# Kernel tuning notes

Measured on AMD Instinct MI355X. Metric: run time of the kernel, lower is better.

Reference implementation:

```python
import jax, jax.numpy as jnp
import numpy as np

LEVELS = 100
TIMESTAMPS = 32768
DIM = 2048
N = 32768
SIG_MIN, SIG_MAX = -3.0, 3.0


def _bipolar(key, shape):
    return jnp.where(jax.random.uniform(key, shape) < 0.5, -1.0, 1.0).astype(jnp.float32)


def setup_inputs() -> dict:
    key = jax.random.key(0)
    ks = jax.random.split(key, 11)
    # (t, x, y, z): sorted times in [0, TIMESTAMPS), gaussian signals
    times = jnp.sort(jax.random.uniform(ks[0], (N,), minval=0.0, maxval=float(TIMESTAMPS)))
    # ensure strictly increasing so jerk dt != 0
    times = times + jnp.arange(N, dtype=jnp.float32) * 1e-3
    xyz = jax.random.normal(ks[1], (N, 3), dtype=jnp.float32)
    inp = jnp.concatenate([times[:, None], xyz], axis=1)  # [N,4]
    return {
        "input": inp,
        "W_x": _bipolar(ks[2], (LEVELS, DIM)),
        "W_y": _bipolar(ks[3], (LEVELS, DIM)),
        "W_z": _bipolar(ks[4], (LEVELS, DIM)),
        "W_mag": _bipolar(ks[5], (LEVELS, DIM)),
        "W_xj": _bipolar(ks[6], (LEVELS, DIM)),
        "W_yj": _bipolar(ks[7], (LEVELS, DIM)),
        "W_zj": _bipolar(ks[8], (LEVELS, DIM)),
        "W_magj": _bipolar(ks[9], (LEVELS, DIM)),
        "W_t": _bipolar(ks[10], (TIMESTAMPS, DIM)),
    }


def _level_lookup(table, value, low, high):
    # torchhd Level: map value in [low, high] to index in [0, n-1], clamp, gather
    n = table.shape[0]
    idx = jnp.round((value - low) / (high - low) * (n - 1)).astype(jnp.int32)
    idx = jnp.clip(idx, 0, n - 1)
    return table[idx]  # [N, DIM]


def reference(input, W_x, W_y, W_z, W_mag, W_xj, W_yj, W_zj, W_magj, W_t):
    t = input[:, 0] - input[0, 0]
    x = jnp.clip(input[:, 1], SIG_MIN, SIG_MAX)
    y = jnp.clip(input[:, 2], SIG_MIN, SIG_MAX)
    z = jnp.clip(input[:, 3], SIG_MIN, SIG_MAX)
    x_lv = _level_lookup(W_x, x, SIG_MIN, SIG_MAX)
    y_lv = _level_lookup(W_y, y, SIG_MIN, SIG_MAX)
    z_lv = _level_lookup(W_z, z, SIG_MIN, SIG_MAX)
    mags = jnp.sqrt(jnp.sum(input[:, 1:] ** 2, axis=1))
    mag_lv = _level_lookup(W_mag, mags, SIG_MIN, SIG_MAX)
    # vectorized jerk: row 0 is zeros (matches the original's initial zeros row)
    dt = t[1:] - t[:-1]
    jerk = jnp.concatenate(
        [jnp.zeros((1, 3), input.dtype), (input[1:, 1:] - input[:-1, 1:]) / dt[:, None]],
        axis=0,
    )  # [N,3]
    xj = jnp.clip(jerk[:, 0], SIG_MIN, SIG_MAX)
    yj = jnp.clip(jerk[:, 1], SIG_MIN, SIG_MAX)
    zj = jnp.clip(jerk[:, 2], SIG_MIN, SIG_MAX)
    xj_lv = _level_lookup(W_xj, xj, SIG_MIN, SIG_MAX)
    yj_lv = _level_lookup(W_yj, yj, SIG_MIN, SIG_MAX)
    zj_lv = _level_lookup(W_zj, zj, SIG_MIN, SIG_MAX)
    jmag = jnp.sqrt(jnp.sum(jerk ** 2, axis=1))
    jmag_lv = _level_lookup(W_magj, jmag, SIG_MIN, SIG_MAX)
    t_lv = _level_lookup(W_t, t, 0.0, float(TIMESTAMPS))
    sample_hvs = ((x_lv + y_lv + z_lv) * mag_lv + (xj_lv + yj_lv + zj_lv) * jmag_lv) * t_lv
    return jnp.tanh(jnp.sum(sample_hvs, axis=0))  # [DIM] multiset + tanh
```

## Files before the change

### kernel.cpp

```cpp
#include <hip/hip_runtime.h>
#include <hip/hip_bf16.h>
#include <math.h>

#define DIM     2048
#define LEVELS  100
#define TSN     32768
#define NSPLIT  32

__device__ __forceinline__ int lvl100(float v) {
    float f = ((v + 3.0f) / 6.0f) * 99.0f;
    int k = (int)rintf(f);
    return min(max(k, 0), LEVELS - 1);
}

__global__ __launch_bounds__(256) void pack_k(
    const float* __restrict__ w0, const float* __restrict__ w1,
    const float* __restrict__ w2, const float* __restrict__ w3,
    const float* __restrict__ w4, const float* __restrict__ w5,
    const float* __restrict__ w6, const float* __restrict__ w7,
    unsigned char* __restrict__ packed)
{
    int blk = blockIdx.x;
    int tb  = blk / LEVELS;
    int lvl = blk - tb * LEVELS;
    const float* w;
    switch (tb) {
        case 0: w = w0; break; case 1: w = w1; break;
        case 2: w = w2; break; case 3: w = w3; break;
        case 4: w = w4; break; case 5: w = w5; break;
        case 6: w = w6; break; default: w = w7; break;
    }
    int t = threadIdx.x;
    const float* p = w + (size_t)lvl * DIM + t * 8;
    float4 a = *(const float4*)p;
    float4 b = *(const float4*)(p + 4);
    unsigned int byte =
        (a.x < 0.f ?   1u : 0u) | (a.y < 0.f ?   2u : 0u) |
        (a.z < 0.f ?   4u : 0u) | (a.w < 0.f ?   8u : 0u) |
        (b.x < 0.f ?  16u : 0u) | (b.y < 0.f ?  32u : 0u) |
        (b.z < 0.f ?  64u : 0u) | (b.w < 0.f ? 128u : 0u);
    packed[(size_t)tb * (LEVELS * 256) + lvl * 256 + t] = (unsigned char)byte;
}

__global__ __launch_bounds__(256) void idx_k(
    const float* __restrict__ inp,
    unsigned long long* __restrict__ sidx,
    unsigned int* __restrict__ tidx, int n)
{
    int i = blockIdx.x * 256 + threadIdx.x;
    if (i >= n) return;
    float t0 = inp[0];
    float ti = inp[i * 4] - t0;
    float x = inp[i * 4 + 1], y = inp[i * 4 + 2], z = inp[i * 4 + 3];
    float xc = fminf(fmaxf(x, -3.f), 3.f);
    float yc = fminf(fmaxf(y, -3.f), 3.f);
    float zc = fminf(fmaxf(z, -3.f), 3.f);
    unsigned long long ix = (unsigned long long)lvl100(xc);
    unsigned long long iy = (unsigned long long)lvl100(yc);
    unsigned long long iz = (unsigned long long)lvl100(zc);
    float mag = sqrtf((x * x + y * y) + z * z);
    unsigned long long im = (unsigned long long)lvl100(mag);
    float jx = 0.f, jy = 0.f, jz = 0.f;
    if (i > 0) {
        float tp = inp[(i - 1) * 4] - t0;
        float dt = ti - tp;
        jx = (x - inp[(i - 1) * 4 + 1]) / dt;
        jy = (y - inp[(i - 1) * 4 + 2]) / dt;
        jz = (z - inp[(i - 1) * 4 + 3]) / dt;
    }
    unsigned long long ixj = (unsigned long long)lvl100(fminf(fmaxf(jx, -3.f), 3.f));
    unsigned long long iyj = (unsigned long long)lvl100(fminf(fmaxf(jy, -3.f), 3.f));
    unsigned long long izj = (unsigned long long)lvl100(fminf(fmaxf(jz, -3.f), 3.f));
    float jm = sqrtf((jx * jx + jy * jy) + jz * jz);
    unsigned long long imj = (unsigned long long)lvl100(jm);
    sidx[i] = ix | (iy << 8) | (iz << 16) | (im << 24) |
              (ixj << 32) | (iyj << 40) | (izj << 48) | (imj << 56);
    float ft = (ti / 32768.0f) * 32767.0f;
    int k = (int)rintf(ft);
    tidx[i] = (unsigned int)min(max(k, 0), TSN - 1);
}

__global__ __launch_bounds__(256) void main_k(
    const float* __restrict__ Wt,
    const unsigned char* __restrict__ packed,
    const unsigned long long* __restrict__ sidx,
    const unsigned int* __restrict__ tidx,
    float* __restrict__ partials, int spb, int n)
{
    const int tid = threadIdx.x;
    const int d0 = tid * 8;
    int s0 = blockIdx.x * spb;
    int s1 = min(s0 + spb, n);
    float acc[8] = {0.f, 0.f, 0.f, 0.f, 0.f, 0.f, 0.f, 0.f};
    for (int s = s0; s < s1; ++s) {
        unsigned long long sp = sidx[s];
        unsigned int ti = tidx[s];
        const float* row = Wt + (size_t)ti * DIM + d0;
        float4 wlo = *(const float4*)row;
        float4 whi = *(const float4*)(row + 4);
        unsigned int i_x  = (unsigned int)(sp)       & 0xffu;
        unsigned int i_y  = (unsigned int)(sp >> 8)  & 0xffu;
        unsigned int i_z  = (unsigned int)(sp >> 16) & 0xffu;
        unsigned int i_m  = (unsigned int)(sp >> 24) & 0xffu;
        unsigned int i_xj = (unsigned int)(sp >> 32) & 0xffu;
        unsigned int i_yj = (unsigned int)(sp >> 40) & 0xffu;
        unsigned int i_zj = (unsigned int)(sp >> 48) & 0xffu;
        unsigned int i_mj = (unsigned int)(sp >> 56) & 0xffu;
        unsigned int Bx  = packed[0 * (LEVELS * 256) + i_x  * 256 + tid];
        unsigned int By  = packed[1 * (LEVELS * 256) + i_y  * 256 + tid];
        unsigned int Bz  = packed[2 * (LEVELS * 256) + i_z  * 256 + tid];
        unsigned int Bm  = packed[3 * (LEVELS * 256) + i_m  * 256 + tid];
        unsigned int Bxj = packed[4 * (LEVELS * 256) + i_xj * 256 + tid];
        unsigned int Byj = packed[5 * (LEVELS * 256) + i_yj * 256 + tid];
        unsigned int Bzj = packed[6 * (LEVELS * 256) + i_zj * 256 + tid];
        unsigned int Bmj = packed[7 * (LEVELS * 256) + i_mj * 256 + tid];
        unsigned int e1 = Bx ^ Bm,  e2 = By ^ Bm,  e3 = Bz ^ Bm;
        unsigned int e4 = Bxj ^ Bmj, e5 = Byj ^ Bmj, e6 = Bzj ^ Bmj;
        unsigned int ta  = e1 ^ e2;
        unsigned int sA  = ta ^ e3;
        unsigned int cA  = (e1 & e2) | (e3 & ta);
        unsigned int tb2 = e4 ^ e5;
        unsigned int sB  = tb2 ^ e6;
        unsigned int cB  = (e4 & e5) | (e6 & tb2);
        unsigned int ones  = sA ^ sB;
        unsigned int cc    = sA & sB;
        unsigned int tc    = cA ^ cB;
        unsigned int twos  = tc ^ cc;
        unsigned int fours = (cA & cB) | (cc & tc);
        float wv[8] = {wlo.x, wlo.y, wlo.z, wlo.w, whi.x, whi.y, whi.z, whi.w};
        #pragma unroll
        for (int j = 0; j < 8; ++j) {
            int v = ((ones >> j) & 1) + 2 * ((twos >> j) & 1) + 4 * ((fours >> j) & 1);
            acc[j] = fmaf((float)(6 - 2 * v), wv[j], acc[j]);
        }
    }
    float* pout = partials + (size_t)blockIdx.x * DIM + d0;
    *(float4*)pout       = make_float4(acc[0], acc[1], acc[2], acc[3]);
    *(float4*)(pout + 4) = make_float4(acc[4], acc[5], acc[6], acc[7]);
}

__global__ __launch_bounds__(256) void reduce1_k(
    const float* __restrict__ partials, float* __restrict__ partial2,
    int rows_per, int nblk)
{
    int d = blockIdx.x * 256 + threadIdx.x;
    int r0 = blockIdx.y * rows_per;
    int r1 = min(r0 + rows_per, nblk);
    float s = 0.f;
    for (int b = r0; b < r1; ++b) s += partials[(size_t)b * DIM + d];
    partial2[(size_t)blockIdx.y * DIM + d] = s;
}

__global__ __launch_bounds__(256) void reduce2_k(
    const float* __restrict__ partial2, float* __restrict__ out)
{
    int d = blockIdx.x * 256 + threadIdx.x;
    float s = 0.f;
    #pragma unroll
    for (int b = 0; b < NSPLIT; ++b) s += partial2[(size_t)b * DIM + d];
    out[d] = tanhf(s);
}

extern "C" void kernel_launch(void* const* d_in, const int* in_sizes, int n_in,
                              void* d_out, int out_size, void* d_ws, size_t ws_size,
                              hipStream_t stream)
{
    const float* inp = (const float*)d_in[0];
    const float* wx  = (const float*)d_in[1];
    const float* wy  = (const float*)d_in[2];
    const float* wz  = (const float*)d_in[3];
    const float* wm  = (const float*)d_in[4];
    const float* wxj = (const float*)d_in[5];
    const float* wyj = (const float*)d_in[6];
    const float* wzj = (const float*)d_in[7];
    const float* wmj = (const float*)d_in[8];
    const float* wt  = (const float*)d_in[9];
    int n = in_sizes[0] / 4;

    char* ws = (char*)d_ws;
    unsigned char* packed = (unsigned char*)ws;
    size_t off = 256 * 1024;
    unsigned long long* sidx = (unsigned long long*)(ws + off);
    off += (size_t)n * 8;
    unsigned int* tidx = (unsigned int*)(ws + off);
    off += (size_t)n * 4;
    off = (off + 255) & ~(size_t)255;

    float* partial2 = (float*)(ws + off);
    off += (size_t)NSPLIT * DIM * 4;

    int nblk = 1024;
    while (nblk > 32 && off + (size_t)nblk * DIM * 4 > ws_size) nblk >>= 1;
    float* partials = (float*)(ws + off);

    hipLaunchKernelGGL(pack_k, dim3(8 * LEVELS), dim3(256), 0, stream,
                       wx, wy, wz, wm, wxj, wyj, wzj, wmj, packed);
    hipLaunchKernelGGL(idx_k, dim3((n + 255) / 256), dim3(256), 0, stream,
                       inp, sidx, tidx, n);
    int spb = (n + nblk - 1) / nblk;
    hipLaunchKernelGGL(main_k, dim3(nblk), dim3(256), 0, stream,
                       wt, packed, sidx, tidx, partials, spb, n);
    int rows_per = (nblk + NSPLIT - 1) / NSPLIT;
    hipLaunchKernelGGL(reduce1_k, dim3(DIM / 256, NSPLIT), dim3(256), 0, stream,
                       partials, partial2, rows_per, nblk);
    hipLaunchKernelGGL(reduce2_k, dim3(DIM / 256), dim3(256), 0, stream,
                       partial2, (float*)d_out);
}
```

Measured before the change: 58.55 us.

## Merge pack and index kernels, make each wavefront own a sample subset

Fuses the bit-packing and index computation into one launch. The packed tables become 32-bit words per lane (64 lanes cover the 2048 dims), and each wavefront now handles its own slice of samples across the full DIM. Wt rows are read as coalesced float4 strided by lane, and the four wavefronts are reduced in shared memory before the partial is written. The aim is fewer launches, wider gather loads and scalar (readfirstlane) sample indices, at the cost of a 32KB LDS buffer and a block-wide sync.

```diff
diff --git a/kernel.cpp b/kernel.cpp
--- a/kernel.cpp
+++ b/kernel.cpp
@@ -6,6 +6,8 @@
 #define LEVELS  100
 #define TSN     32768
 #define NSPLIT  32
+#define NBLK    1024
+#define PACK_BLOCKS 200
 
 __device__ __forceinline__ int lvl100(float v) {
     float f = ((v + 3.0f) / 6.0f) * 99.0f;
@@ -13,41 +15,42 @@
     return min(max(k, 0), LEVELS - 1);
 }
 
-__global__ __launch_bounds__(256) void pack_k(
+__global__ __launch_bounds__(256) void prep_k(
     const float* __restrict__ w0, const float* __restrict__ w1,
     const float* __restrict__ w2, const float* __restrict__ w3,
     const float* __restrict__ w4, const float* __restrict__ w5,
     const float* __restrict__ w6, const float* __restrict__ w7,
-    unsigned char* __restrict__ packed)
-{
-    int blk = blockIdx.x;
-    int tb  = blk / LEVELS;
-    int lvl = blk - tb * LEVELS;
-    const float* w;
-    switch (tb) {
-        case 0: w = w0; break; case 1: w = w1; break;
-        case 2: w = w2; break; case 3: w = w3; break;
-        case 4: w = w4; break; case 5: w = w5; break;
-        case 6: w = w6; break; default: w = w7; break;
-    }
-    int t = threadIdx.x;
-    const float* p = w + (size_t)lvl * DIM + t * 8;
-    float4 a = *(const float4*)p;
-    float4 b = *(const float4*)(p + 4);
-    unsigned int byte =
-        (a.x < 0.f ?   1u : 0u) | (a.y < 0.f ?   2u : 0u) |
-        (a.z < 0.f ?   4u : 0u) | (a.w < 0.f ?   8u : 0u) |
-        (b.x < 0.f ?  16u : 0u) | (b.y < 0.f ?  32u : 0u) |
-        (b.z < 0.f ?  64u : 0u) | (b.w < 0.f ? 128u : 0u);
-    packed[(size_t)tb * (LEVELS * 256) + lvl * 256 + t] = (unsigned char)byte;
-}
-
-__global__ __launch_bounds__(256) void idx_k(
     const float* __restrict__ inp,
+    unsigned int* __restrict__ packed2,
     unsigned long long* __restrict__ sidx,
     unsigned int* __restrict__ tidx, int n)
 {
-    int i = blockIdx.x * 256 + threadIdx.x;
+    if (blockIdx.x < PACK_BLOCKS) {
+        int tab = blockIdx.x / 25;
+        int lg  = blockIdx.x - tab * 25;
+        int l   = threadIdx.x & 63;
+        int level = lg * 4 + (threadIdx.x >> 6);
+        const float* w;
+        switch (tab) {
+            case 0: w = w0; break; case 1: w = w1; break;
+            case 2: w = w2; break; case 3: w = w3; break;
+            case 4: w = w4; break; case 5: w = w5; break;
+            case 6: w = w6; break; default: w = w7; break;
+        }
+        const float* base = w + (size_t)level * DIM + 4 * l;
+        unsigned int word = 0;
+        #pragma unroll
+        for (int k = 0; k < 8; ++k) {
+            float4 a = *(const float4*)(base + 256 * k);
+            word |= (a.x < 0.f ? 1u : 0u) << (4 * k);
+            word |= (a.y < 0.f ? 1u : 0u) << (4 * k + 1);
+            word |= (a.z < 0.f ? 1u : 0u) << (4 * k + 2);
+            word |= (a.w < 0.f ? 1u : 0u) << (4 * k + 3);
+        }
+        packed2[(tab * LEVELS + level) * 64 + l] = word;
+        return;
+    }
+    int i = (blockIdx.x - PACK_BLOCKS) * 256 + threadIdx.x;
     if (i >= n) return;
     float t0 = inp[0];
     float ti = inp[i * 4] - t0;
@@ -82,22 +85,29 @@
 
 __global__ __launch_bounds__(256) void main_k(
     const float* __restrict__ Wt,
-    const unsigned char* __restrict__ packed,
+    const unsigned int* __restrict__ packed2,
     const unsigned long long* __restrict__ sidx,
     const unsigned int* __restrict__ tidx,
-    float* __restrict__ partials, int spb, int n)
-{
+    float* __restrict__ partials, int spw, int n)
+{
+    __shared__ float red[4][DIM];
     const int tid = threadIdx.x;
-    const int d0 = tid * 8;
-    int s0 = blockIdx.x * spb;
-    int s1 = min(s0 + spb, n);
-    float acc[8] = {0.f, 0.f, 0.f, 0.f, 0.f, 0.f, 0.f, 0.f};
+    const int l   = tid & 63;
+    const int wv  = tid >> 6;
+    int gw = blockIdx.x * 4 + wv;
+    int s0 = gw * spw;
+    int s1 = min(s0 + spw, n);
+
+    float4 acc[8];
+    #pragma unroll
+    for (int k = 0; k < 8; ++k) acc[k] = make_float4(0.f, 0.f, 0.f, 0.f);
+
     for (int s = s0; s < s1; ++s) {
-        unsigned long long sp = sidx[s];
-        unsigned int ti = tidx[s];
-        const float* row = Wt + (size_t)ti * DIM + d0;
-        float4 wlo = *(const float4*)row;
-        float4 whi = *(const float4*)(row + 4);
+        int su = __builtin_amdgcn_readfirstlane(s);
+        unsigned long long sp = sidx[su];
+        unsigned int ti = tidx[su];
+        const float4* rowp = (const float4*)(Wt + (size_t)ti * DIM);
+
         unsigned int i_x  = (unsigned int)(sp)       & 0xffu;
         unsigned int i_y  = (unsigned int)(sp >> 8)  & 0xffu;
         unsigned int i_z  = (unsigned int)(sp >> 16) & 0xffu;
@@ -106,14 +116,16 @@
         unsigned int i_yj = (unsigned int)(sp >> 40) & 0xffu;
         unsigned int i_zj = (unsigned int)(sp >> 48) & 0xffu;
         unsigned int i_mj = (unsigned int)(sp >> 56) & 0xffu;
-        unsigned int Bx  = packed[0 * (LEVELS * 256) + i_x  * 256 + tid];
-        unsigned int By  = packed[1 * (LEVELS * 256) + i_y  * 256 + tid];
-        unsigned int Bz  = packed[2 * (LEVELS * 256) + i_z  * 256 + tid];
-        unsigned int Bm  = packed[3 * (LEVELS * 256) + i_m  * 256 + tid];
-        unsigned int Bxj = packed[4 * (LEVELS * 256) + i_xj * 256 + tid];
-        unsigned int Byj = packed[5 * (LEVELS * 256) + i_yj * 256 + tid];
-        unsigned int Bzj = packed[6 * (LEVELS * 256) + i_zj * 256 + tid];
-        unsigned int Bmj = packed[7 * (LEVELS * 256) + i_mj * 256 + tid];
+
+        unsigned int Bx  = packed2[(0 * LEVELS + i_x ) * 64 + l];
+        unsigned int By  = packed2[(1 * LEVELS + i_y ) * 64 + l];
+        unsigned int Bz  = packed2[(2 * LEVELS + i_z ) * 64 + l];
+        unsigned int Bm  = packed2[(3 * LEVELS + i_m ) * 64 + l];
+        unsigned int Bxj = packed2[(4 * LEVELS + i_xj) * 64 + l];
+        unsigned int Byj = packed2[(5 * LEVELS + i_yj) * 64 + l];
+        unsigned int Bzj = packed2[(6 * LEVELS + i_zj) * 64 + l];
+        unsigned int Bmj = packed2[(7 * LEVELS + i_mj) * 64 + l];
+
         unsigned int e1 = Bx ^ Bm,  e2 = By ^ Bm,  e3 = Bz ^ Bm;
         unsigned int e4 = Bxj ^ Bmj, e5 = Byj ^ Bmj, e6 = Bzj ^ Bmj;
         unsigned int ta  = e1 ^ e2;
@@ -127,16 +139,40 @@
         unsigned int tc    = cA ^ cB;
         unsigned int twos  = tc ^ cc;
         unsigned int fours = (cA & cB) | (cc & tc);
-        float wv[8] = {wlo.x, wlo.y, wlo.z, wlo.w, whi.x, whi.y, whi.z, whi.w};
+
         #pragma unroll
-        for (int j = 0; j < 8; ++j) {
-            int v = ((ones >> j) & 1) + 2 * ((twos >> j) & 1) + 4 * ((fours >> j) & 1);
-            acc[j] = fmaf((float)(6 - 2 * v), wv[j], acc[j]);
+        for (int k = 0; k < 8; ++k) {
+            float4 wt4 = rowp[64 * k + l];
+            #pragma unroll
+            for (int j = 0; j < 4; ++j) {
+                int p = 4 * k + j;
+                int v = ((ones >> p) & 1) + 2 * ((twos >> p) & 1)
+                      + 4 * ((fours >> p) & 1);
+                float sgn = (float)(6 - 2 * v);
+                float* a = (float*)&acc[k];
+                float* wf = (float*)&wt4;
+                a[j] = fmaf(sgn, wf[j], a[j]);
+            }
         }
     }
-    float* pout = partials + (size_t)blockIdx.x * DIM + d0;
-    *(float4*)pout       = make_float4(acc[0], acc[1], acc[2], acc[3]);
-    *(float4*)(pout + 4) = make_float4(acc[4], acc[5], acc[6], acc[7]);
+
+    float4* redw = (float4*)red[wv];
+    #pragma unroll
+    for (int k = 0; k < 8; ++k) redw[64 * k + l] = acc[k];
+    __syncthreads();
+
+    float4 o0 = make_float4(0.f, 0.f, 0.f, 0.f);
+    float4 o1 = make_float4(0.f, 0.f, 0.f, 0.f);
+    #pragma unroll
+    for (int r = 0; r < 4; ++r) {
+        float4 a = ((float4*)red[r])[2 * tid];
+        float4 b = ((float4*)red[r])[2 * tid + 1];
+        o0.x += a.x; o0.y += a.y; o0.z += a.z; o0.w += a.w;
+        o1.x += b.x; o1.y += b.y; o1.z += b.z; o1.w += b.w;
+    }
+    float4* pout = (float4*)(partials + (size_t)blockIdx.x * DIM + tid * 8);
+    pout[0] = o0;
+    pout[1] = o1;
 }
 
 __global__ __launch_bounds__(256) void reduce1_k(
@@ -178,7 +214,7 @@
     int n = in_sizes[0] / 4;
 
     char* ws = (char*)d_ws;
-    unsigned char* packed = (unsigned char*)ws;
+    unsigned int* packed2 = (unsigned int*)ws;
     size_t off = 256 * 1024;
     unsigned long long* sidx = (unsigned long long*)(ws + off);
     off += (size_t)n * 8;
@@ -189,17 +225,17 @@
     float* partial2 = (float*)(ws + off);
     off += (size_t)NSPLIT * DIM * 4;
 
-    int nblk = 1024;
+    int nblk = NBLK;
     while (nblk > 32 && off + (size_t)nblk * DIM * 4 > ws_size) nblk >>= 1;
     float* partials = (float*)(ws + off);
 
-    hipLaunchKernelGGL(pack_k, dim3(8 * LEVELS), dim3(256), 0, stream,
-                       wx, wy, wz, wm, wxj, wyj, wzj, wmj, packed);
-    hipLaunchKernelGGL(idx_k, dim3((n + 255) / 256), dim3(256), 0, stream,
-                       inp, sidx, tidx, n);
-    int spb = (n + nblk - 1) / nblk;
+    int idx_blocks = (n + 255) / 256;
+    hipLaunchKernelGGL(prep_k, dim3(PACK_BLOCKS + idx_blocks), dim3(256), 0, stream,
+                       wx, wy, wz, wm, wxj, wyj, wzj, wmj,
+                       inp, packed2, sidx, tidx, n);
+    int spw = (n + nblk * 4 - 1) / (nblk * 4);
     hipLaunchKernelGGL(main_k, dim3(nblk), dim3(256), 0, stream,
-                       wt, packed, sidx, tidx, partials, spb, n);
+                       wt, packed2, sidx, tidx, partials, spw, n);
     int rows_per = (nblk + NSPLIT - 1) / NSPLIT;
     hipLaunchKernelGGL(reduce1_k, dim3(DIM / 256, NSPLIT), dim3(256), 0, stream,
                        partials, partial2, rows_per, nblk);
```

Result: faster. 55.10 us (-5.9%).
